# Optimization experiments

Hardware: AMD Instinct MI355X
Metric: run time of the kernel (lower is better)

Reference implementation:

```python
import jax, jax.numpy as jnp
import numpy as np

B, S, E, H = 8, 1024, 64, 8
DK = E // H  # n_wires per head
DIM = 2 ** DK  # statevector size


def _quantum_projection(x, phi):
    """Faithful batched simulation of _QLayer for every (batch, seq, head).
    Encoder RX(x_i) followed by trainable RX(phi_i) on the same wire equals
    RX(x_i + phi_i). Then a CNOT ring, then <Z_w> for each wire.
    x: [B,S,E] float, phi: [H,DK] float -> [B,S,E] float expectations.
    """
    b, s, e = x.shape
    theta = x.reshape(b, s, H, DK) + phi  # [B,S,H,DK]
    M = b * s * H
    th = theta.reshape(M, DK)
    # RX(t)|0> = cos(t/2)|0> - i sin(t/2)|1>
    c = jnp.cos(th * 0.5).astype(jnp.complex64)
    sn = (jnp.sin(th * 0.5) * (-1j)).astype(jnp.complex64)
    q = jnp.stack([c, sn], axis=-1)  # [M, DK, 2]
    # product state via iterated kron over the DK wires (fixed small loop)
    amps = jnp.ones((M, 1), jnp.complex64)
    for w in range(DK):
        amps = (amps[:, :, None] * q[:, w, None, :]).reshape(M, -1)
    st = amps.reshape((M,) + (2,) * DK)
    # CNOT ring: (0,1),(1,2),...,(DK-2,DK-1),(DK-1,0)
    gates = [(w, w + 1) for w in range(DK - 1)] + [(DK - 1, 0)]
    for cw, tw in gates:
        ac = 1 + cw
        s0 = jnp.take(st, 0, axis=ac)  # control = 0: identity
        s1 = jnp.take(st, 1, axis=ac)  # control = 1: flip target
        at = 1 + tw - (1 if tw > cw else 0)  # target axis after removing control axis
        s1 = jnp.flip(s1, axis=at)
        st = jnp.stack([s0, s1], axis=ac)
    stf = st.reshape(M, DIM)
    probs = stf.real ** 2 + stf.imag ** 2  # [M, DIM]
    # <Z_w> = sum_k probs[k] * (1 - 2*bit_w(k)); wire 0 is most-significant bit
    bits = (jnp.arange(DIM)[:, None] >> jnp.arange(DK - 1, -1, -1)[None, :]) & 1
    signs = (1 - 2 * bits).astype(probs.dtype)  # [DIM, DK]
    expz = probs @ signs  # [M, DK]
    return expz.reshape(b, s, e)


def setup_inputs() -> dict:
    key = jax.random.key(0)
    k1, k2, k3, k4 = jax.random.split(key, 4)
    x = jax.random.normal(k1, (B, S, E), dtype=jnp.float32)
    phi = jax.random.normal(k2, (H, DK), dtype=jnp.float32) * 0.1  # trainable RX params
    lim = 1.0 / np.sqrt(E)
    W = jax.random.uniform(k3, (E, E), jnp.float32, -lim, lim)  # combine Linear weight
    b = jax.random.uniform(k4, (E,), jnp.float32, -lim, lim)    # combine Linear bias
    return {"x": x, "phi": phi, "W": W, "b": b}


def reference(x, phi, W, b):
    # q = k = v = _projection(x): the original calls _projection(x) 3 times with
    # the same params and no randomness, so they are identical; compute once.
    proj = _quantum_projection(x, phi)  # [B,S,E]
    scores = jax.nn.softmax(
        jnp.einsum('bse,bte->bst', proj, proj) / jnp.sqrt(jnp.float32(DK)), axis=-1)
    # dropout is identity in eval mode
    ctx = jnp.einsum('bst,bte->bse', scores, proj)
    return ctx @ W.T + b
```

## Files before the change

kernel.cpp:

```cpp
#include <hip/hip_runtime.h>
#include <hip/hip_bf16.h>

#define BB 8
#define SS 1024
#define EE 64
#define HH 8
#define DKW 8

typedef __hip_bfloat16 bf16;
typedef unsigned short u16;
typedef _Float16 half8v __attribute__((ext_vector_type(8)));
typedef float floatx4 __attribute__((ext_vector_type(4)));

#define MFMA16(a, b, c) __builtin_amdgcn_mfma_f32_16x16x32_f16(a, b, c, 0, 0, 0)

#define OFF_PROJT ((size_t)BB * SS * EE * 2)

template <int NT>
__device__ __forceinline__ bool detect_f32(const u16* __restrict__ base,
                                           int tid, int* red) {
    int cnt = 0;
    for (int i = tid; i < 2048; i += NT) {
        u16 u = base[i * 2];
        int ex = (u >> 7) & 0xFF;
        cnt += (ex >= 0x84) ? 1 : 0;
    }
#pragma unroll
    for (int off = 32; off > 0; off >>= 1) cnt += __shfl_xor(cnt, off, 64);
    if ((tid & 63) == 0) red[tid >> 6] = cnt;
    __syncthreads();
    int tot = 0;
#pragma unroll
    for (int w = 0; w < NT / 64; ++w) tot += red[w];
    return tot > 64;
}

__device__ __forceinline__ void proj_compute(const void* x, const void* phi,
                                             bool f32, int m, float* z) {
    int h = m & (HH - 1);
    float th[DKW];
    if (f32) {
        const float4* xp = (const float4*)((const float*)x + (size_t)m * DKW);
        const float4* pp = (const float4*)((const float*)phi + h * DKW);
        float4 x0 = xp[0], x1 = xp[1];
        float4 p0 = pp[0], p1 = pp[1];
        th[0] = x0.x + p0.x; th[1] = x0.y + p0.y; th[2] = x0.z + p0.z; th[3] = x0.w + p0.w;
        th[4] = x1.x + p1.x; th[5] = x1.y + p1.y; th[6] = x1.z + p1.z; th[7] = x1.w + p1.w;
    } else {
        union { uint4 u; bf16 hv[8]; } xu, pu;
        xu.u = *(const uint4*)((const bf16*)x + (size_t)m * DKW);
        pu.u = *(const uint4*)((const bf16*)phi + (size_t)h * DKW);
#pragma unroll
        for (int j = 0; j < DKW; ++j)
            th[j] = __bfloat162float(xu.hv[j]) + __bfloat162float(pu.hv[j]);
    }
    float c[DKW];
#pragma unroll
    for (int j = 0; j < DKW; ++j) c[j] = __cosf(th[j]);
    float suf = c[1];
#pragma unroll
    for (int j = 2; j < DKW; ++j) suf *= c[j];
    z[0] = suf;
    float pre = c[0];
#pragma unroll
    for (int w = 1; w < DKW; ++w) { pre *= c[w]; z[w] = pre; }
}

__global__ __launch_bounds__(256) void proj_f16_kernel(const void* __restrict__ x,
                                                       const void* __restrict__ phi,
                                                       _Float16* __restrict__ projH,
                                                       _Float16* __restrict__ projT) {
    __shared__ int redd[4];
    __shared__ _Float16 zt[EE][40];
    const int tid = threadIdx.x;
    const bool f32 = detect_f32<256>((const u16*)x, tid, redd);

    const int m = blockIdx.x * 256 + tid;
    float z[DKW];
    proj_compute(x, phi, f32, m, z);

    union { half8v v; _Float16 h[8]; } o;
#pragma unroll
    for (int j = 0; j < DKW; ++j) o.h[j] = (_Float16)z[j];
    *(half8v*)(projH + (size_t)m * DKW) = o.v;

    const int h = m & (HH - 1);
    const int sl = (tid >> 3) & 31;
#pragma unroll
    for (int j = 0; j < DKW; ++j) zt[h * DKW + j][sl] = o.h[j];
    __syncthreads();

    const int b = blockIdx.x >> 5;
    const int s0 = (blockIdx.x * 32) & (SS - 1);
    const int row = tid >> 2, ch = tid & 3;
    half8v vv = *(const half8v*)(&zt[row][ch * 8]);
    *(half8v*)(projT + ((size_t)(b * EE + row)) * SS + s0 + ch * 8) = vv;
}

__device__ __forceinline__ int sidx(int row, int colblk) {
    return row * 1024 + ((colblk ^ (row & 7)) << 3);
}

__global__ __launch_bounds__(512) void fused_attn(const _Float16* __restrict__ projH,
                                                  const _Float16* __restrict__ projT,
                                                  const void* __restrict__ Wp,
                                                  const void* __restrict__ biasp,
                                                  void* __restrict__ outp) {
    __shared__ _Float16 Stile[32 * 1024];
    __shared__ float    pacc[4][32][17];
    __shared__ _Float16 ctx_lds[32][72];
    __shared__ float    rowsum[32];
    __shared__ int      redd[8];

    const int tid = threadIdx.x;
    const int wave = tid >> 6, lane = tid & 63;
    const int lr = lane & 15, quad = lane >> 4;
    const int bid = blockIdx.x;
    const int b = bid & 7;
    const int m0 = (bid >> 3) * 32;

    const bool f32 = detect_f32<512>((const u16*)Wp, tid, redd);

    const int o_out = (wave & 3) * 16 + lr;
    half8v wb0, wb1;
    float bo;
    {
        if (f32) {
            const float* wr = (const float*)Wp + (size_t)o_out * EE;
            union { half8v v; _Float16 h[8]; } w0, w1;
#pragma unroll
            for (int j = 0; j < 8; ++j) {
                w0.h[j] = (_Float16)wr[quad * 8 + j];
                w1.h[j] = (_Float16)wr[32 + quad * 8 + j];
            }
            wb0 = w0.v; wb1 = w1.v;
            bo = ((const float*)biasp)[o_out];
        } else {
            const bf16* wr = (const bf16*)Wp + (size_t)o_out * EE;
            union { uint4 u; bf16 hv[8]; } r0, r1;
            r0.u = *(const uint4*)(wr + quad * 8);
            r1.u = *(const uint4*)(wr + 32 + quad * 8);
            union { half8v v; _Float16 h[8]; } w0, w1;
#pragma unroll
            for (int j = 0; j < 8; ++j) {
                w0.h[j] = (_Float16)__bfloat162float(r0.hv[j]);
                w1.h[j] = (_Float16)__bfloat162float(r1.hv[j]);
            }
            wb0 = w0.v; wb1 = w1.v;
            bo = __bfloat162float(((const bf16*)biasp)[o_out]);
        }
    }

    const _Float16* Pb = projH + (size_t)b * SS * EE;
    const float scale = 0.35355339059327373f;

    {
        const _Float16* ar0 = Pb + (size_t)(m0 + lr) * EE;
        const _Float16* ar1 = Pb + (size_t)(m0 + 16 + lr) * EE;
        half8v a0 = *(const half8v*)(ar0 + quad * 8);
        half8v a1 = *(const half8v*)(ar0 + 32 + quad * 8);
        half8v a2 = *(const half8v*)(ar1 + quad * 8);
        half8v a3 = *(const half8v*)(ar1 + 32 + quad * 8);
#pragma unroll 2
        for (int c = 0; c < 8; ++c) {
            int n = wave * 128 + c * 16;
            const _Float16* brow = Pb + (size_t)(n + lr) * EE;
            half8v b0 = *(const half8v*)(brow + quad * 8);
            half8v b1 = *(const half8v*)(brow + 32 + quad * 8);
            floatx4 acc0 = {0.f, 0.f, 0.f, 0.f};
            floatx4 acc1 = {0.f, 0.f, 0.f, 0.f};
            acc0 = MFMA16(a0, b0, acc0);
            acc0 = MFMA16(a1, b1, acc0);
            acc1 = MFMA16(a2, b0, acc1);
            acc1 = MFMA16(a3, b1, acc1);
            int colblk = (n + lr) >> 3, cin = (n + lr) & 7;
#pragma unroll
            for (int r = 0; r < 4; ++r) {
                Stile[sidx(quad * 4 + r, colblk) + cin]      = (_Float16)(acc0[r] * scale);
                Stile[sidx(16 + quad * 4 + r, colblk) + cin] = (_Float16)(acc1[r] * scale);
            }
        }
    }
    __syncthreads();

    {
        const int row = tid >> 4, seg = tid & 15;
        half8v hv[8];
#pragma unroll
        for (int i = 0; i < 8; ++i)
            hv[i] = *(const half8v*)(&Stile[sidx(row, i * 16 + seg)]);
        float mloc = -1e30f;
#pragma unroll
        for (int i = 0; i < 8; ++i)
#pragma unroll
            for (int j = 0; j < 8; ++j) mloc = fmaxf(mloc, (float)hv[i][j]);
#pragma unroll
        for (int off = 8; off > 0; off >>= 1)
            mloc = fmaxf(mloc, __shfl_xor(mloc, off, 64));
        float lsum = 0.f;
#pragma unroll
        for (int i = 0; i < 8; ++i) {
#pragma unroll
            for (int j = 0; j < 8; ++j) {
                float e = __expf((float)hv[i][j] - mloc);
                lsum += e;
                hv[i][j] = (_Float16)(e * 256.f);
            }
        }
#pragma unroll
        for (int off = 8; off > 0; off >>= 1)
            lsum += __shfl_xor(lsum, off, 64);
        if (seg == 0) rowsum[row] = lsum;
#pragma unroll
        for (int i = 0; i < 8; ++i)
            *(half8v*)(&Stile[sidx(row, i * 16 + seg)]) = hv[i];
    }
    __syncthreads();

    const int kh = wave >> 2, eg = wave & 3;
    {
        const int e = eg * 16 + lr;
        const _Float16* vrow = projT + ((size_t)(b * EE + e)) * SS + kh * 512;
        floatx4 acc0 = {0.f, 0.f, 0.f, 0.f};
        floatx4 acc1 = {0.f, 0.f, 0.f, 0.f};
#pragma unroll 4
        for (int k0 = 0; k0 < 512; k0 += 32) {
            int kb = ((kh * 512 + k0) >> 3) + quad;
            half8v B  = *(const half8v*)(vrow + k0 + quad * 8);
            half8v A0 = *(const half8v*)(&Stile[sidx(lr, kb)]);
            half8v A1 = *(const half8v*)(&Stile[sidx(16 + lr, kb)]);
            acc0 = MFMA16(A0, B, acc0);
            acc1 = MFMA16(A1, B, acc1);
        }
        if (kh == 1) {
#pragma unroll
            for (int r = 0; r < 4; ++r) {
                pacc[eg][quad * 4 + r][lr]      = acc0[r];
                pacc[eg][16 + quad * 4 + r][lr] = acc1[r];
            }
        }
        __syncthreads();
        if (kh == 0) {
#pragma unroll
            for (int r = 0; r < 4; ++r) {
                int r0 = quad * 4 + r, r1 = 16 + quad * 4 + r;
                float inv0 = 1.0f / (256.0f * rowsum[r0]);
                float inv1 = 1.0f / (256.0f * rowsum[r1]);
                ctx_lds[r0][e] = (_Float16)((acc0[r] + pacc[eg][r0][lr]) * inv0);
                ctx_lds[r1][e] = (_Float16)((acc1[r] + pacc[eg][r1][lr]) * inv1);
            }
        }
    }
    __syncthreads();

    {
        const int rowg = wave >> 2;
        half8v ca0 = *(const half8v*)(&ctx_lds[rowg * 16 + lr][quad * 8]);
        half8v ca1 = *(const half8v*)(&ctx_lds[rowg * 16 + lr][32 + quad * 8]);
        floatx4 oacc = {0.f, 0.f, 0.f, 0.f};
        oacc = MFMA16(ca0, wb0, oacc);
        oacc = MFMA16(ca1, wb1, oacc);
#pragma unroll
        for (int r = 0; r < 4; ++r) {
            size_t oi = ((size_t)b * SS + m0 + rowg * 16 + quad * 4 + r) * EE + o_out;
            float val = oacc[r] + bo;
            if (f32) ((float*)outp)[oi] = val;
            else     ((bf16*)outp)[oi] = __float2bfloat16(val);
        }
    }
}

extern "C" void kernel_launch(void* const* d_in, const int* in_sizes, int n_in,
                              void* d_out, int out_size, void* d_ws, size_t ws_size,
                              hipStream_t stream) {
    const void* x    = d_in[0];
    const void* phi  = d_in[1];
    const void* W    = d_in[2];
    const void* bias = d_in[3];

    _Float16* projH = (_Float16*)d_ws;
    _Float16* projT = (_Float16*)((char*)d_ws + OFF_PROJT);

    proj_f16_kernel<<<dim3(BB * SS * HH / 256), dim3(256), 0, stream>>>(x, phi, projH, projT);
    fused_attn<<<dim3(256), dim3(512), 0, stream>>>(projH, projT, W, bias, d_out);
}
```

Measured before the change: 78.43 us.

## Fuse projection into attention kernel with grid-wide atomic barrier

Merges the quantum projection kernel into the attention kernel. Each block computes its own 32-row slice of projH/projT, then all blocks wait at a software grid barrier built on an atomic counter before attention starts. This removes one kernel launch and the gap between the two kernels, but adds a memset call and a spin-wait. It also relies on all 256 blocks being resident at the same time, otherwise the barrier deadlocks. The f32 dtype check now reads x instead of W.

```diff
diff --git a/kernel.cpp b/kernel.cpp
--- a/kernel.cpp
+++ b/kernel.cpp
@@ -15,6 +15,7 @@
 #define MFMA16(a, b, c) __builtin_amdgcn_mfma_f32_16x16x32_f16(a, b, c, 0, 0, 0)
 
 #define OFF_PROJT ((size_t)BB * SS * EE * 2)
+#define OFF_CNT   ((size_t)2 * BB * SS * EE * 2)
 
 template <int NT>
 __device__ __forceinline__ bool detect_f32(const u16* __restrict__ base,
@@ -66,46 +67,18 @@
     for (int w = 1; w < DKW; ++w) { pre *= c[w]; z[w] = pre; }
 }
 
-__global__ __launch_bounds__(256) void proj_f16_kernel(const void* __restrict__ x,
-                                                       const void* __restrict__ phi,
-                                                       _Float16* __restrict__ projH,
-                                                       _Float16* __restrict__ projT) {
-    __shared__ int redd[4];
-    __shared__ _Float16 zt[EE][40];
-    const int tid = threadIdx.x;
-    const bool f32 = detect_f32<256>((const u16*)x, tid, redd);
-
-    const int m = blockIdx.x * 256 + tid;
-    float z[DKW];
-    proj_compute(x, phi, f32, m, z);
-
-    union { half8v v; _Float16 h[8]; } o;
-#pragma unroll
-    for (int j = 0; j < DKW; ++j) o.h[j] = (_Float16)z[j];
-    *(half8v*)(projH + (size_t)m * DKW) = o.v;
-
-    const int h = m & (HH - 1);
-    const int sl = (tid >> 3) & 31;
-#pragma unroll
-    for (int j = 0; j < DKW; ++j) zt[h * DKW + j][sl] = o.h[j];
-    __syncthreads();
-
-    const int b = blockIdx.x >> 5;
-    const int s0 = (blockIdx.x * 32) & (SS - 1);
-    const int row = tid >> 2, ch = tid & 3;
-    half8v vv = *(const half8v*)(&zt[row][ch * 8]);
-    *(half8v*)(projT + ((size_t)(b * EE + row)) * SS + s0 + ch * 8) = vv;
-}
-
 __device__ __forceinline__ int sidx(int row, int colblk) {
     return row * 1024 + ((colblk ^ (row & 7)) << 3);
 }
 
-__global__ __launch_bounds__(512) void fused_attn(const _Float16* __restrict__ projH,
-                                                  const _Float16* __restrict__ projT,
-                                                  const void* __restrict__ Wp,
-                                                  const void* __restrict__ biasp,
-                                                  void* __restrict__ outp) {
+__global__ __launch_bounds__(512) void qattn(const void* __restrict__ x,
+                                             const void* __restrict__ phi,
+                                             const void* __restrict__ Wp,
+                                             const void* __restrict__ biasp,
+                                             void* __restrict__ outp,
+                                             _Float16* __restrict__ projH,
+                                             _Float16* __restrict__ projT,
+                                             unsigned int* __restrict__ cnt) {
     __shared__ _Float16 Stile[32 * 1024];
     __shared__ float    pacc[4][32][17];
     __shared__ _Float16 ctx_lds[32][72];
@@ -119,7 +92,7 @@
     const int b = bid & 7;
     const int m0 = (bid >> 3) * 32;
 
-    const bool f32 = detect_f32<512>((const u16*)Wp, tid, redd);
+    const bool f32 = detect_f32<512>((const u16*)x, tid, redd);
 
     const int o_out = (wave & 3) * 16 + lr;
     half8v wb0, wb1;
@@ -150,6 +123,36 @@
             bo = __bfloat162float(((const bf16*)biasp)[o_out]);
         }
     }
+
+    {
+        _Float16 (*zt)[40] = (_Float16 (*)[40])Stile;
+        if (tid < 256) {
+            int s_local = tid >> 3, h = tid & 7;
+            int m = ((b << 10) + m0 + s_local) * 8 + h;
+            float z[DKW];
+            proj_compute(x, phi, f32, m, z);
+            union { half8v v; _Float16 hx[8]; } o;
+#pragma unroll
+            for (int j = 0; j < DKW; ++j) o.hx[j] = (_Float16)z[j];
+            *(half8v*)(projH + (size_t)m * DKW) = o.v;
+#pragma unroll
+            for (int j = 0; j < DKW; ++j) zt[h * DKW + j][s_local] = o.hx[j];
+        }
+        __syncthreads();
+        if (tid < 256) {
+            int row = tid >> 2, ch = tid & 3;
+            half8v vv = *(const half8v*)(&zt[row][ch * 8]);
+            *(half8v*)(projT + ((size_t)(b * EE + row)) * SS + m0 + ch * 8) = vv;
+        }
+    }
+    __threadfence();
+    __syncthreads();
+    if (tid == 0) {
+        __hip_atomic_fetch_add(cnt, 1u, __ATOMIC_ACQ_REL, __HIP_MEMORY_SCOPE_AGENT);
+        while (__hip_atomic_load(cnt, __ATOMIC_ACQUIRE, __HIP_MEMORY_SCOPE_AGENT)
+               < (unsigned)gridDim.x) { __builtin_amdgcn_s_sleep(8); }
+    }
+    __syncthreads();
 
     const _Float16* Pb = projH + (size_t)b * SS * EE;
     const float scale = 0.35355339059327373f;
@@ -280,7 +283,9 @@
 
     _Float16* projH = (_Float16*)d_ws;
     _Float16* projT = (_Float16*)((char*)d_ws + OFF_PROJT);
-
-    proj_f16_kernel<<<dim3(BB * SS * HH / 256), dim3(256), 0, stream>>>(x, phi, projH, projT);
-    fused_attn<<<dim3(256), dim3(512), 0, stream>>>(projH, projT, W, bias, d_out);
-}
+    unsigned int* cnt = (unsigned int*)((char*)d_ws + OFF_CNT);
+
+    hipMemsetAsync(cnt, 0, sizeof(unsigned int), stream);
+    qattn<<<dim3(256), dim3(512), 0, stream>>>(x, phi, W, bias, d_out,
+                                               projH, projT, cnt);
+}
```

New measurement: 121.3 us. 54.6% more time.
